# Optimization experiments

Measured on AMD Instinct MI355X. Metric: run time of the kernel, lower is better.

Reference implementation:

```python
import jax, jax.numpy as jnp
import numpy as np
import math

N, E, G = 10000, 100000, 500
HID, H = 128, 4
C = HID                      # out_channels per head (PyG TransformerConv)
NFREQ, NSPACE = 10, 3
EDIM = 2 * NFREQ * NSPACE    # 60 = dis_emb.dim
LAT, DIS = 6, 3
IN_DIM = HID + LAT + DIS     # 137
EPS = 1e-5


def _lin_init(k, fan_in, shape):
    b = 1.0 / math.sqrt(fan_in)
    return jax.random.uniform(k, shape, jnp.float32, -b, b)


def setup_inputs() -> dict:
    key = jax.random.key(0)
    ks = jax.random.split(key, 12)
    return dict(
        node_features=jax.random.normal(ks[0], (N, HID), jnp.float32),
        frac_coords=jax.random.uniform(ks[1], (N, DIS), jnp.float32),
        lattice_feats=jax.random.normal(ks[2], (G, LAT), jnp.float32),
        edge_index=jax.random.randint(ks[3], (2, E), 0, N),
        node2graph=jnp.sort(jax.random.randint(ks[4], (N,), 0, G)),
        frac_diff=jax.random.normal(ks[5], (E, DIS), jnp.float32) * 0.1,
        ln_gamma=jnp.ones((HID,), jnp.float32),
        ln_beta=jnp.zeros((HID,), jnp.float32),
        Wq=_lin_init(ks[6], IN_DIM, (IN_DIM, H * C)), bq=jnp.zeros((H * C,), jnp.float32),
        Wk=_lin_init(ks[7], IN_DIM, (IN_DIM, H * C)), bk=jnp.zeros((H * C,), jnp.float32),
        Wv=_lin_init(ks[8], IN_DIM, (IN_DIM, H * C)), bv=jnp.zeros((H * C,), jnp.float32),
        We=_lin_init(ks[9], EDIM, (EDIM, H * C)),
        Wskip=_lin_init(ks[10], IN_DIM, (IN_DIM, C)), bskip=jnp.zeros((C,), jnp.float32),
    )


def _sinusoids(frac_diff):
    # SinusoidsEmbedding: emb = x[...,None]*2*pi*arange(F); cat(sin, cos); detached
    freqs = 2.0 * jnp.pi * jnp.arange(NFREQ, dtype=jnp.float32)    # [F]
    emb = frac_diff[:, :, None] * freqs[None, None, :]             # [E,3,F]
    emb = emb.reshape(-1, NSPACE * NFREQ)                          # [E,30]
    return jnp.concatenate([jnp.sin(emb), jnp.cos(emb)], axis=-1)  # [E,60]


def _segment_softmax(scores, idx, num_segments):
    # softmax over variable-size neighborhoods grouped by target node idx
    m = jax.ops.segment_max(scores, idx, num_segments=num_segments)
    ex = jnp.exp(scores - m[idx])
    s = jax.ops.segment_sum(ex, idx, num_segments=num_segments)
    return ex / (s[idx] + 1e-16)


def reference(node_features, frac_coords, lattice_feats, edge_index, node2graph,
              frac_diff, ln_gamma, ln_beta, Wq, bq, Wk, bk, Wv, bv, We, Wskip, bskip):
    edge_emb = jax.lax.stop_gradient(_sinusoids(frac_diff))  # .detach() in original
    node_input = node_features
    # LayerNorm (biased variance, torch default)
    mu = node_features.mean(-1, keepdims=True)
    var = node_features.var(-1, keepdims=True)
    h = (node_features - mu) * jax.lax.rsqrt(var + EPS) * ln_gamma + ln_beta
    # gather per-graph lattice features to nodes, concat
    lat = lattice_feats.reshape(-1, LAT)[node2graph]                # [N,6]
    x = jnp.concatenate([h, lat, frac_coords], axis=1)              # [N,137]

    q = (x @ Wq + bq).reshape(N, H, C)
    k = (x @ Wk + bk).reshape(N, H, C)
    v = (x @ Wv + bv).reshape(N, H, C)
    e = (edge_emb @ We).reshape(E, H, C)                            # lin_edge (no bias)

    src, dst = edge_index[0], edge_index[1]  # message flows src -> dst (PyG default)
    k_e = k[src] + e                                                # [E,H,C]
    alpha = (q[dst] * k_e).sum(-1) / math.sqrt(C)                   # [E,H]
    alpha = _segment_softmax(alpha, dst, N)
    msg = (v[src] + e) * alpha[:, :, None]                          # [E,H,C]
    out = jax.ops.segment_sum(msg, dst, num_segments=N)             # [N,H,C]
    out = out.mean(axis=1)                                          # concat=False -> head mean
    out = out + (x @ Wskip + bskip)                                 # root skip connection
    return node_input + jax.nn.silu(out)
```

## Files before the change

kernel.cpp:

```cpp
#include <hip/hip_runtime.h>
#include <math.h>

#define N_NODES 10000
#define N_EDGES 100000
#define HIDDEN  128
#define NHEAD   4
#define CHAN    128
#define IN_DIM  137
#define KPAD    160
#define NCOLS   1904
#define NPAD    1920
#define LATD    6
#define DISD    3

#define PREP_BLOCKS 2500
#define TRANS_TILES 26
#define WQE_BLOCKS  150
#define WEBT_BLOCKS 128

#define SCAT_BLOCKS ((N_EDGES + 255) / 256)
#define GEMM_BX 15
#define GEMM_BY ((N_NODES + 63) / 64)

typedef __attribute__((ext_vector_type(8))) short short8v;
typedef __attribute__((ext_vector_type(4))) float float4v;
typedef __attribute__((ext_vector_type(2))) float float2v;

__device__ inline unsigned short f2bf(float f) {
    unsigned u = __float_as_uint(f);
    unsigned r = 0x7fffu + ((u >> 16) & 1u);
    return (unsigned short)((u + r) >> 16);
}
__device__ inline float bf2f(unsigned short u) {
    return __uint_as_float(((unsigned)u) << 16);
}

__global__ __launch_bounds__(256) void prep_weights_kernel(
    const float* __restrict__ nf, const float* __restrict__ frac,
    const float* __restrict__ lat, const int* __restrict__ n2g,
    const float* __restrict__ gamma, const float* __restrict__ beta,
    const float* __restrict__ Wq, const float* __restrict__ bq,
    const float* __restrict__ Wk, const float* __restrict__ bk,
    const float* __restrict__ Wv, const float* __restrict__ bv,
    const float* __restrict__ Wsk, const float* __restrict__ bsk,
    const float* __restrict__ We,
    unsigned short* __restrict__ xb, int* __restrict__ hist,
    unsigned short* __restrict__ wallT, float* __restrict__ bias_all,
    unsigned short* __restrict__ webt)
{
    __shared__ __align__(16) unsigned short Tlds[64 * 168];
    const int tid = threadIdx.x;

    if (blockIdx.x < PREP_BLOCKS) {
        int wave = tid >> 6;
        int lane = tid & 63;
        int n = blockIdx.x * 4 + wave;
        if (n >= N_NODES) return;

        float v0 = nf[n * HIDDEN + lane];
        float v1 = nf[n * HIDDEN + 64 + lane];
        float s  = v0 + v1;
        float sq = v0 * v0 + v1 * v1;
        #pragma unroll
        for (int m = 1; m < 64; m <<= 1) {
            s  += __shfl_xor(s, m);
            sq += __shfl_xor(sq, m);
        }
        float mean = s * (1.0f / 128.0f);
        float var  = sq * (1.0f / 128.0f) - mean * mean;
        float inv  = rsqrtf(var + 1e-5f);

        xb[n * KPAD + lane]      = f2bf((v0 - mean) * inv * gamma[lane]      + beta[lane]);
        xb[n * KPAD + 64 + lane] = f2bf((v1 - mean) * inv * gamma[64 + lane] + beta[64 + lane]);
        if (lane < LATD) xb[n * KPAD + HIDDEN + lane]        = f2bf(lat[n2g[n] * LATD + lane]);
        if (lane < DISD) xb[n * KPAD + HIDDEN + LATD + lane] = f2bf(frac[n * DISD + lane]);
        if (lane >= 41)  xb[n * KPAD + 96 + lane] = 0;
        if (lane == 0)   hist[n] = 0;
    } else if (blockIdx.x < PREP_BLOCKS + TRANS_TILES) {
        const int n0 = (blockIdx.x - PREP_BLOCKS) * 64;
        for (int i = tid; i < 160 * 64; i += 256) {
            const int k = i >> 6, n = i & 63;
            const int col = n0 + n;
            float val = 0.0f;
            if (k < IN_DIM) {
                if (col < 512)        val = Wq[(size_t)k * 512 + col];
                else if (col < 1024)  val = Wk[(size_t)k * 512 + (col - 512)];
                else if (col < 1536)  val = Wv[(size_t)k * 512 + (col - 1024)];
                else                  val = Wsk[(size_t)k * 128 + (col - 1536)];
            }
            Tlds[n * 168 + k] = f2bf(val);
        }
        __syncthreads();
        for (int i = tid; i < 64 * 20; i += 256) {
            const int n = i / 20, c8 = (i % 20) * 8;
            *reinterpret_cast<uint4*>(&wallT[(size_t)(n0 + n) * KPAD + c8]) =
                *reinterpret_cast<const uint4*>(&Tlds[n * 168 + c8]);
        }
        if (tid < 64) {
            const int col = n0 + tid;
            float b;
            if (col < 512)        b = bq[col];
            else if (col < 1024)  b = bk[col - 512];
            else if (col < 1536)  b = bv[col - 1024];
            else                  b = bsk[col - 1536];
            bias_all[col] = b;
        }
    } else if (blockIdx.x < PREP_BLOCKS + TRANS_TILES + WQE_BLOCKS) {
        int idx = (blockIdx.x - PREP_BLOCKS - TRANS_TILES) * 256 + tid;
        if (idx >= 240 * KPAD) return;
        int hj = idx / KPAD, k = idx % KPAD;
        int h = hj / 60, j = hj % 60;
        float s = 0.0f;
        if (k < IN_DIM) {
            #pragma unroll 4
            for (int c = 0; c < 128; ++c)
                s += Wq[(size_t)k * 512 + h * 128 + c] * We[(size_t)j * 512 + h * 128 + c];
        }
        wallT[(size_t)(1664 + hj) * KPAD + k] = f2bf(s);
        if (k == KPAD - 1) {
            float b = 0.0f;
            #pragma unroll 4
            for (int c = 0; c < 128; ++c)
                b += bq[h * 128 + c] * We[(size_t)j * 512 + h * 128 + c];
            bias_all[1664 + hj] = b;
        }
    } else {
        int g = (blockIdx.x - PREP_BLOCKS - TRANS_TILES - WQE_BLOCKS) * 256 + tid;
        if (g >= 4 * 128 * 64) return;
        int h = g >> 13, c = (g >> 6) & 127, j = g & 63;
        float v = (j < 60) ? We[(size_t)j * 512 + h * 128 + c] : 0.0f;
        webt[g] = f2bf(v);
    }
}

__global__ __launch_bounds__(256) void hist_kernel(
    const int* __restrict__ eidx, int* __restrict__ hist)
{
    int e = blockIdx.x * 256 + threadIdx.x;
    if (e < N_EDGES) atomicAdd(&hist[eidx[N_EDGES + e]], 1);
}

__global__ __launch_bounds__(1024) void scan_kernel(
    const int* __restrict__ hist, int* __restrict__ offsets, int* __restrict__ cursor)
{
    __shared__ int part[1024];
    const int t = threadIdx.x;
    const int base = t * 10;
    int loc[10];
    int s = 0;
    #pragma unroll
    for (int i = 0; i < 10; ++i) {
        int v = (base + i < N_NODES) ? hist[base + i] : 0;
        loc[i] = s; s += v;
    }
    part[t] = s;
    __syncthreads();
    for (int off = 1; off < 1024; off <<= 1) {
        int v = (t >= off) ? part[t - off] : 0;
        __syncthreads();
        part[t] += v;
        __syncthreads();
    }
    int pre = (t > 0) ? part[t - 1] : 0;
    #pragma unroll
    for (int i = 0; i < 10; ++i)
        if (base + i < N_NODES) {
            offsets[base + i] = pre + loc[i];
            cursor[base + i]  = pre + loc[i];
        }
    if (t == 1023) offsets[N_NODES] = part[1023];
}

__global__ __launch_bounds__(256) void gemm_scatter_kernel(
    const unsigned short* __restrict__ xb, const unsigned short* __restrict__ wallT,
    const float* __restrict__ bias_all,
    const int* __restrict__ eidx, const float* __restrict__ fdiff,
    int* __restrict__ cursor, int* __restrict__ sorted_src,
    float* __restrict__ sorted_fd,
    float* __restrict__ sq, unsigned short* __restrict__ qbuf,
    unsigned char* __restrict__ kvb)
{
    __shared__ __align__(16) unsigned short Alds[64 * 168];

    if (blockIdx.x < SCAT_BLOCKS) {
        int e = blockIdx.x * 256 + threadIdx.x;
        if (e >= N_EDGES) return;
        int src = eidx[e];
        int dst = eidx[N_EDGES + e];
        int pos = atomicAdd(&cursor[dst], 1);
        sorted_src[pos] = src;
        sorted_fd[pos * 3 + 0] = fdiff[e * 3 + 0];
        sorted_fd[pos * 3 + 1] = fdiff[e * 3 + 1];
        sorted_fd[pos * 3 + 2] = fdiff[e * 3 + 2];
        return;
    }

    const int bx   = blockIdx.x - SCAT_BLOCKS;
    const int row0 = (bx / GEMM_BX) * 64;
    const int col0 = (bx % GEMM_BX) * 128;
    const int tid  = threadIdx.x;

    for (int i = tid; i < 64 * 20; i += 256) {
        int r = i / 20, c8 = (i % 20) * 8;
        uint4 v = make_uint4(0u, 0u, 0u, 0u);
        if (row0 + r < N_NODES)
            v = *reinterpret_cast<const uint4*>(&xb[(size_t)(row0 + r) * KPAD + c8]);
        *reinterpret_cast<uint4*>(&Alds[r * 168 + c8]) = v;
    }
    __syncthreads();

    const int l   = tid & 63;
    const int wid = tid >> 6;
    const int wr  = (wid >> 1) * 32;
    const int wc  = (wid & 1) * 64;
    const int lr  = l & 15;
    const int lk  = (l >> 4) * 8;

    float4v acc[2][4];
    #pragma unroll
    for (int tr = 0; tr < 2; ++tr)
        #pragma unroll
        for (int tc = 0; tc < 4; ++tc)
            acc[tr][tc] = (float4v){0.0f, 0.0f, 0.0f, 0.0f};

    #pragma unroll
    for (int ks = 0; ks < 5; ++ks) {
        short8v a[2], b[4];
        #pragma unroll
        for (int t = 0; t < 2; ++t)
            a[t] = *reinterpret_cast<const short8v*>(&Alds[(wr + t * 16 + lr) * 168 + ks * 32 + lk]);
        #pragma unroll
        for (int t = 0; t < 4; ++t)
            b[t] = *reinterpret_cast<const short8v*>(
                &wallT[(size_t)(col0 + wc + t * 16 + lr) * KPAD + ks * 32 + lk]);
        #pragma unroll
        for (int tr = 0; tr < 2; ++tr)
            #pragma unroll
            for (int tc = 0; tc < 4; ++tc)
                acc[tr][tc] = __builtin_amdgcn_mfma_f32_16x16x32_bf16(a[tr], b[tc], acc[tr][tc], 0, 0, 0);
    }

    #pragma unroll
    for (int tr = 0; tr < 2; ++tr) {
        #pragma unroll
        for (int tc = 0; tc < 4; ++tc) {
            const int col  = col0 + wc + tc * 16 + lr;
            const float bias = bias_all[col];
            #pragma unroll
            for (int j = 0; j < 4; ++j) {
                const int row = row0 + wr + tr * 16 + (l >> 4) * 4 + j;
                if (row < N_NODES) {
                    float val = acc[tr][tc][j] + bias;
                    if (col < 512) {
                        qbuf[(size_t)row * 512 + col] = f2bf(val);
                    } else if (col < 1024) {
                        const int h = (col - 512) >> 7, ck = (col - 512) & 127;
                        int p = __builtin_amdgcn_cvt_pk_fp8_f32(val, val, 0, false);
                        kvb[((size_t)row * 4 + h) * 256 + ck] = (unsigned char)(p & 0xFF);
                    } else if (col < 1536) {
                        const int h = (col - 1024) >> 7, cv = (col - 1024) & 127;
                        int p = __builtin_amdgcn_cvt_pk_fp8_f32(val, val, 0, false);
                        kvb[((size_t)row * 4 + h) * 256 + 128 + cv] = (unsigned char)(p & 0xFF);
                    } else if (col < 1664) {
                        sq[(size_t)row * 384 + (col - 1536)] = val;
                    } else if (col < NCOLS) {
                        sq[(size_t)row * 384 + 128 + (col - 1664)] = val;
                    }
                }
            }
        }
    }
}

__global__ __launch_bounds__(256) void gather_kernel(
    const float* __restrict__ sq, const unsigned short* __restrict__ qbuf,
    const unsigned char* __restrict__ kvb,
    const int* __restrict__ offsets, const int* __restrict__ sorted_src,
    const float* __restrict__ sorted_fd,
    float* __restrict__ avbuf, unsigned short* __restrict__ aggbuf,
    float* __restrict__ sumwbuf)
{
    const int n    = blockIdx.x;
    const int h    = threadIdx.x >> 6;
    const int l    = threadIdx.x & 63;
    const int hl   = l & 31;
    const int half = l >> 5;
    const float TWO_PI = 6.283185307179586f;
    const float scale  = 0.08838834764831845f;

    const ushort4 qv = *reinterpret_cast<const ushort4*>(
        &qbuf[(size_t)n * 512 + h * 128 + 4 * hl]);
    const float q4x = bf2f(qv.x), q4y = bf2f(qv.y);
    const float q4z = bf2f(qv.z), q4w = bf2f(qv.w);
    const float qe_a = sq[(size_t)n * 384 + 128 + h * 60 + hl];
    const bool  v2ok = (hl < 28);
    const float qe_b = v2ok ? sq[(size_t)n * 384 + 128 + h * 60 + hl + 32] : 0.0f;

    const int   jj1  = (hl < 30) ? hl : hl - 30;
    const int   sd1  = jj1 / 10;
    const float fc1  = TWO_PI * (float)(jj1 % 10);
    const bool  sin1 = (hl < 30);
    const int   jj2  = hl + 2;
    const int   sd2  = v2ok ? (jj2 / 10) : 0;
    const float fc2  = v2ok ? TWO_PI * (float)(jj2 % 10) : 0.0f;

    float ax = 0.f, ay = 0.f, az = 0.f, aw = 0.f;
    float agg1 = 0.f, agg2 = 0.f, sumw = 0.f;
    const int e0 = offsets[n], e1 = offsets[n + 1];

    for (int base = e0; base < e1; base += 4) {
        const int eA = base + half;
        const int eB = base + half + 2;
        const bool okA = (eA < e1), okB = (eB < e1);
        const int iA = okA ? eA : e0;
        const int iB = okB ? eB : e0;
        const int srcA = sorted_src[iA];
        const int srcB = sorted_src[iB];
        const float fdA1 = sorted_fd[iA * 3 + sd1];
        const float fdA2 = sorted_fd[iA * 3 + sd2];
        const float fdB1 = sorted_fd[iB * 3 + sd1];
        const float fdB2 = sorted_fd[iB * 3 + sd2];
        const unsigned char* pA = kvb + ((size_t)srcA * 4 + h) * 256;
        const unsigned char* pB = kvb + ((size_t)srcB * 4 + h) * 256;
        const unsigned kAu = *reinterpret_cast<const unsigned*>(pA + 4 * hl);
        const unsigned vAu = *reinterpret_cast<const unsigned*>(pA + 128 + 4 * hl);
        const unsigned kBu = *reinterpret_cast<const unsigned*>(pB + 4 * hl);
        const unsigned vBu = *reinterpret_cast<const unsigned*>(pB + 128 + 4 * hl);

        const float eA1 = sin1 ? __sinf(fdA1 * fc1) : __cosf(fdA1 * fc1);
        const float eA2 = __cosf(fdA2 * fc2);
        const float eB1 = sin1 ? __sinf(fdB1 * fc1) : __cosf(fdB1 * fc1);
        const float eB2 = __cosf(fdB2 * fc2);

        const float2v kA01 = __builtin_amdgcn_cvt_pk_f32_fp8(kAu, false);
        const float2v kA23 = __builtin_amdgcn_cvt_pk_f32_fp8(kAu, true);
        const float2v kB01 = __builtin_amdgcn_cvt_pk_f32_fp8(kBu, false);
        const float2v kB23 = __builtin_amdgcn_cvt_pk_f32_fp8(kBu, true);

        float pAs = q4x * kA01[0] + q4y * kA01[1]
                  + q4z * kA23[0] + q4w * kA23[1]
                  + eA1 * qe_a + eA2 * qe_b;
        float pBs = q4x * kB01[0] + q4y * kB01[1]
                  + q4z * kB23[0] + q4w * kB23[1]
                  + eB1 * qe_a + eB2 * qe_b;
        #pragma unroll
        for (int m = 1; m <= 16; m <<= 1) {
            pAs += __shfl_xor(pAs, m);
            pBs += __shfl_xor(pBs, m);
        }
        const float wA = okA ? __expf(pAs * scale) : 0.0f;
        const float wB = okB ? __expf(pBs * scale) : 0.0f;
        sumw += wA + wB;

        const float2v vA01 = __builtin_amdgcn_cvt_pk_f32_fp8(vAu, false);
        const float2v vA23 = __builtin_amdgcn_cvt_pk_f32_fp8(vAu, true);
        const float2v vB01 = __builtin_amdgcn_cvt_pk_f32_fp8(vBu, false);
        const float2v vB23 = __builtin_amdgcn_cvt_pk_f32_fp8(vBu, true);
        ax += wA * vA01[0] + wB * vB01[0];
        ay += wA * vA01[1] + wB * vB01[1];
        az += wA * vA23[0] + wB * vB23[0];
        aw += wA * vA23[1] + wB * vB23[1];
        agg1 += wA * eA1 + wB * eB1;
        if (v2ok) agg2 += wA * eA2 + wB * eB2;
    }

    sumw += __shfl_xor(sumw, 32);
    ax += __shfl_xor(ax, 32);  ay += __shfl_xor(ay, 32);
    az += __shfl_xor(az, 32);  aw += __shfl_xor(aw, 32);
    agg1 += __shfl_xor(agg1, 32);
    agg2 += __shfl_xor(agg2, 32);

    if (half == 0) {
        float4 r;
        r.x = ax; r.y = ay; r.z = az; r.w = aw;
        *reinterpret_cast<float4*>(&avbuf[(size_t)n * 512 + h * 128 + 4 * hl]) = r;
        aggbuf[n * 256 + h * 64 + hl]      = f2bf(agg1);
        aggbuf[n * 256 + h * 64 + 32 + hl] = f2bf(agg2);
        if (hl == 0) sumwbuf[n * 4 + h] = sumw;
    }
}

__global__ __launch_bounds__(256) void corrfin_kernel(
    const unsigned short* __restrict__ webt, const unsigned short* __restrict__ aggbuf,
    const float* __restrict__ avbuf, const float* __restrict__ sumwbuf,
    const float* __restrict__ sq, const float* __restrict__ nf,
    float* __restrict__ out)
{
    const int node0 = blockIdx.x * 64;
    const int tid = threadIdx.x;
    const int l   = tid & 63;
    const int w   = tid >> 6;
    const int lr  = l & 15;
    const int lk  = (l >> 4) * 8;
    const int nbase = node0 + w * 16;

    float4v acc[4][8];
    #pragma unroll
    for (int h = 0; h < 4; ++h)
        #pragma unroll
        for (int nn = 0; nn < 8; ++nn)
            acc[h][nn] = (float4v){0.0f, 0.0f, 0.0f, 0.0f};

    const int arow = (nbase + lr < N_NODES) ? (nbase + lr) : 0;
    #pragma unroll
    for (int h = 0; h < 4; ++h) {
        #pragma unroll
        for (int ks = 0; ks < 2; ++ks) {
            const short8v a = *reinterpret_cast<const short8v*>(
                &aggbuf[(size_t)arow * 256 + h * 64 + ks * 32 + lk]);
            #pragma unroll
            for (int nn = 0; nn < 8; ++nn) {
                const short8v b = *reinterpret_cast<const short8v*>(
                    &webt[(size_t)(h * 128 + nn * 16 + lr) * 64 + ks * 32 + lk]);
                acc[h][nn] = __builtin_amdgcn_mfma_f32_16x16x32_bf16(a, b, acc[h][nn], 0, 0, 0);
            }
        }
    }

    float inv_sw[4][4];
    #pragma unroll
    for (int j = 0; j < 4; ++j) {
        const int node = nbase + (l >> 4) * 4 + j;
        const int nrd  = (node < N_NODES) ? node : 0;
        #pragma unroll
        for (int h = 0; h < 4; ++h)
            inv_sw[j][h] = 1.0f / (sumwbuf[nrd * 4 + h] + 1e-16f);
    }

    #pragma unroll
    for (int nn = 0; nn < 8; ++nn) {
        const int col = nn * 16 + lr;
        #pragma unroll
        for (int j = 0; j < 4; ++j) {
            const int node = nbase + (l >> 4) * 4 + j;
            if (node < N_NODES) {
                float z = 0.0f;
                #pragma unroll
                for (int h = 0; h < 4; ++h)
                    z += (avbuf[(size_t)node * 512 + h * 128 + col] + acc[h][nn][j])
                         * inv_sw[j][h];
                z = 0.25f * z + sq[(size_t)node * 384 + col];
                float si = z / (1.0f + __expf(-z));
                out[node * CHAN + col] = nf[node * CHAN + col] + si;
            }
        }
    }
}

extern "C" void kernel_launch(void* const* d_in, const int* in_sizes, int n_in,
                              void* d_out, int out_size, void* d_ws, size_t ws_size,
                              hipStream_t stream)
{
    const float* nf    = (const float*)d_in[0];
    const float* frac  = (const float*)d_in[1];
    const float* lat   = (const float*)d_in[2];
    const int*   eidx  = (const int*)  d_in[3];
    const int*   n2g   = (const int*)  d_in[4];
    const float* fdiff = (const float*)d_in[5];
    const float* gamma = (const float*)d_in[6];
    const float* beta  = (const float*)d_in[7];
    const float* Wq    = (const float*)d_in[8];
    const float* bq    = (const float*)d_in[9];
    const float* Wk    = (const float*)d_in[10];
    const float* bk    = (const float*)d_in[11];
    const float* Wv    = (const float*)d_in[12];
    const float* bv    = (const float*)d_in[13];
    const float* We    = (const float*)d_in[14];
    const float* Wsk   = (const float*)d_in[15];
    const float* bsk   = (const float*)d_in[16];
    float* out = (float*)d_out;

    float* sq        = (float*)d_ws;
    float* avbuf     = sq + (size_t)N_NODES * 384;
    float* sumwbuf   = avbuf + (size_t)N_NODES * 512;
    float* bias_all  = sumwbuf + (size_t)N_NODES * 4;
    float* sorted_fd = bias_all + NPAD;
    unsigned short* xb     = (unsigned short*)(sorted_fd + (size_t)N_EDGES * 3);
    unsigned short* wallT  = xb + (size_t)N_NODES * KPAD;
    unsigned short* webt   = wallT + (size_t)NPAD * KPAD;
    unsigned short* aggbuf = webt + 4 * 128 * 64;
    unsigned short* qbuf   = aggbuf + (size_t)N_NODES * 256;
    unsigned char*  kvb    = (unsigned char*)(qbuf + (size_t)N_NODES * 512);
    int* hist       = (int*)(kvb + (size_t)N_NODES * 4 * 256);
    int* offsets    = hist + N_NODES;
    int* cursor     = offsets + N_NODES + 1;
    int* sorted_src = cursor + N_NODES;

    prep_weights_kernel<<<PREP_BLOCKS + TRANS_TILES + WQE_BLOCKS + WEBT_BLOCKS,
                          256, 0, stream>>>(
        nf, frac, lat, n2g, gamma, beta,
        Wq, bq, Wk, bk, Wv, bv, Wsk, bsk, We,
        xb, hist, wallT, bias_all, webt);

    hist_kernel<<<(N_EDGES + 255) / 256, 256, 0, stream>>>(eidx, hist);
    scan_kernel<<<1, 1024, 0, stream>>>(hist, offsets, cursor);

    gemm_scatter_kernel<<<SCAT_BLOCKS + GEMM_BX * GEMM_BY, 256, 0, stream>>>(
        xb, wallT, bias_all, eidx, fdiff, cursor, sorted_src, sorted_fd,
        sq, qbuf, kvb);

    gather_kernel<<<N_NODES, 256, 0, stream>>>(
        sq, qbuf, kvb, offsets, sorted_src, sorted_fd, avbuf, aggbuf, sumwbuf);

    corrfin_kernel<<<(N_NODES + 63) / 64, 256, 0, stream>>>(
        webt, aggbuf, avbuf, sumwbuf, sq, nf, out);
}
```

Measured before the change: 134.3 us.

## Store GEMM operands in MFMA fragment layout and drop LDS staging

The prep kernel now writes the normalized node features and the concatenated weight matrix directly in MFMA 16x16x32 fragment order, so each lane's 8 bf16 values are contiguous. The GEMM kernel loads all A and B fragments straight from global memory into registers with coalesced 16-byte loads. This removes the shared-memory staging pass and its barrier. It also adds a launch-bounds occupancy hint. The cost is higher register pressure from holding all fragments at once, and the node-feature writes in the prep kernel become scattered.

```diff
diff --git a/kernel.cpp b/kernel.cpp
--- a/kernel.cpp
+++ b/kernel.cpp
@@ -21,6 +21,8 @@
 #define SCAT_BLOCKS ((N_EDGES + 255) / 256)
 #define GEMM_BX 15
 #define GEMM_BY ((N_NODES + 63) / 64)
+#define NR16    628
+#define FRAG_STRIDE (5 * 64 * 8)
 
 typedef __attribute__((ext_vector_type(8))) short short8v;
 typedef __attribute__((ext_vector_type(4))) float float4v;
@@ -33,6 +35,13 @@
 }
 __device__ inline float bf2f(unsigned short u) {
     return __uint_as_float(((unsigned)u) << 16);
+}
+__device__ inline size_t frag_off(int grp16, int ks, int lane) {
+    return (((size_t)grp16 * 5 + ks) * 64 + lane) * 8;
+}
+__device__ inline size_t frag_elem(int grp16, int lr, int k) {
+    const int ks = k >> 5, g = (k >> 3) & 3, e = k & 7;
+    return frag_off(grp16, ks, g * 16 + lr) + e;
 }
 
 __global__ __launch_bounds__(256) void prep_weights_kernel(
@@ -44,8 +53,8 @@
     const float* __restrict__ Wv, const float* __restrict__ bv,
     const float* __restrict__ Wsk, const float* __restrict__ bsk,
     const float* __restrict__ We,
-    unsigned short* __restrict__ xb, int* __restrict__ hist,
-    unsigned short* __restrict__ wallT, float* __restrict__ bias_all,
+    unsigned short* __restrict__ xfrag, int* __restrict__ hist,
+    unsigned short* __restrict__ wfrag, float* __restrict__ bias_all,
     unsigned short* __restrict__ webt)
 {
     __shared__ __align__(16) unsigned short Tlds[64 * 168];
@@ -70,12 +79,18 @@
         float var  = sq * (1.0f / 128.0f) - mean * mean;
         float inv  = rsqrtf(var + 1e-5f);
 
-        xb[n * KPAD + lane]      = f2bf((v0 - mean) * inv * gamma[lane]      + beta[lane]);
-        xb[n * KPAD + 64 + lane] = f2bf((v1 - mean) * inv * gamma[64 + lane] + beta[64 + lane]);
-        if (lane < LATD) xb[n * KPAD + HIDDEN + lane]        = f2bf(lat[n2g[n] * LATD + lane]);
-        if (lane < DISD) xb[n * KPAD + HIDDEN + LATD + lane] = f2bf(frac[n * DISD + lane]);
-        if (lane >= 41)  xb[n * KPAD + 96 + lane] = 0;
-        if (lane == 0)   hist[n] = 0;
+        const int r16 = n >> 4, lr = n & 15;
+        xfrag[frag_elem(r16, lr, lane)] =
+            f2bf((v0 - mean) * inv * gamma[lane] + beta[lane]);
+        xfrag[frag_elem(r16, lr, 64 + lane)] =
+            f2bf((v1 - mean) * inv * gamma[64 + lane] + beta[64 + lane]);
+        if (lane < LATD)
+            xfrag[frag_elem(r16, lr, HIDDEN + lane)] = f2bf(lat[n2g[n] * LATD + lane]);
+        if (lane < DISD)
+            xfrag[frag_elem(r16, lr, HIDDEN + LATD + lane)] = f2bf(frac[n * DISD + lane]);
+        if (lane >= 41)
+            xfrag[frag_elem(r16, lr, 96 + lane)] = 0;
+        if (lane == 0) hist[n] = 0;
     } else if (blockIdx.x < PREP_BLOCKS + TRANS_TILES) {
         const int n0 = (blockIdx.x - PREP_BLOCKS) * 64;
         for (int i = tid; i < 160 * 64; i += 256) {
@@ -91,10 +106,16 @@
             Tlds[n * 168 + k] = f2bf(val);
         }
         __syncthreads();
-        for (int i = tid; i < 64 * 20; i += 256) {
-            const int n = i / 20, c8 = (i % 20) * 8;
-            *reinterpret_cast<uint4*>(&wallT[(size_t)(n0 + n) * KPAD + c8]) =
-                *reinterpret_cast<const uint4*>(&Tlds[n * 168 + c8]);
+        for (int i = tid; i < 4 * 5 * 64; i += 256) {
+            const int lane = i & 63;
+            const int ks   = (i >> 6) % 5;
+            const int c16l = i / (5 * 64);
+            const int lr = lane & 15, g = lane >> 4;
+            const int lcol = c16l * 16 + lr;
+            const int k0 = ks * 32 + g * 8;
+            const short8v v = *reinterpret_cast<const short8v*>(&Tlds[lcol * 168 + k0]);
+            *reinterpret_cast<short8v*>(
+                &wfrag[frag_off((n0 >> 4) + c16l, ks, lane)]) = v;
         }
         if (tid < 64) {
             const int col = n0 + tid;
@@ -116,13 +137,14 @@
             for (int c = 0; c < 128; ++c)
                 s += Wq[(size_t)k * 512 + h * 128 + c] * We[(size_t)j * 512 + h * 128 + c];
         }
-        wallT[(size_t)(1664 + hj) * KPAD + k] = f2bf(s);
+        const int col = 1664 + hj;
+        wfrag[frag_elem(col >> 4, col & 15, k)] = f2bf(s);
         if (k == KPAD - 1) {
             float b = 0.0f;
             #pragma unroll 4
             for (int c = 0; c < 128; ++c)
                 b += bq[h * 128 + c] * We[(size_t)j * 512 + h * 128 + c];
-            bias_all[1664 + hj] = b;
+            bias_all[col] = b;
         }
     } else {
         int g = (blockIdx.x - PREP_BLOCKS - TRANS_TILES - WQE_BLOCKS) * 256 + tid;
@@ -171,8 +193,8 @@
     if (t == 1023) offsets[N_NODES] = part[1023];
 }
 
-__global__ __launch_bounds__(256) void gemm_scatter_kernel(
-    const unsigned short* __restrict__ xb, const unsigned short* __restrict__ wallT,
+__global__ __launch_bounds__(256, 2) void gemm_scatter_kernel(
+    const unsigned short* __restrict__ xfrag, const unsigned short* __restrict__ wfrag,
     const float* __restrict__ bias_all,
     const int* __restrict__ eidx, const float* __restrict__ fdiff,
     int* __restrict__ cursor, int* __restrict__ sorted_src,
@@ -180,8 +202,6 @@
     float* __restrict__ sq, unsigned short* __restrict__ qbuf,
     unsigned char* __restrict__ kvb)
 {
-    __shared__ __align__(16) unsigned short Alds[64 * 168];
-
     if (blockIdx.x < SCAT_BLOCKS) {
         int e = blockIdx.x * 256 + threadIdx.x;
         if (e >= N_EDGES) return;
@@ -199,22 +219,26 @@
     const int row0 = (bx / GEMM_BX) * 64;
     const int col0 = (bx % GEMM_BX) * 128;
     const int tid  = threadIdx.x;
-
-    for (int i = tid; i < 64 * 20; i += 256) {
-        int r = i / 20, c8 = (i % 20) * 8;
-        uint4 v = make_uint4(0u, 0u, 0u, 0u);
-        if (row0 + r < N_NODES)
-            v = *reinterpret_cast<const uint4*>(&xb[(size_t)(row0 + r) * KPAD + c8]);
-        *reinterpret_cast<uint4*>(&Alds[r * 168 + c8]) = v;
-    }
-    __syncthreads();
-
-    const int l   = tid & 63;
-    const int wid = tid >> 6;
-    const int wr  = (wid >> 1) * 32;
-    const int wc  = (wid & 1) * 64;
-    const int lr  = l & 15;
-    const int lk  = (l >> 4) * 8;
+    const int l    = tid & 63;
+    const int wid  = tid >> 6;
+    const int wr   = (wid >> 1) * 32;
+    const int wc   = (wid & 1) * 64;
+    const int lr   = l & 15;
+    const int r16  = (row0 + wr) >> 4;
+    const int c16  = (col0 + wc) >> 4;
+
+    short8v a[2][5], b[4][5];
+    #pragma unroll
+    for (int ks = 0; ks < 5; ++ks) {
+        #pragma unroll
+        for (int t = 0; t < 2; ++t)
+            a[t][ks] = *reinterpret_cast<const short8v*>(
+                &xfrag[frag_off(r16 + t, ks, l)]);
+        #pragma unroll
+        for (int t = 0; t < 4; ++t)
+            b[t][ks] = *reinterpret_cast<const short8v*>(
+                &wfrag[frag_off(c16 + t, ks, l)]);
+    }
 
     float4v acc[2][4];
     #pragma unroll
@@ -224,21 +248,13 @@
             acc[tr][tc] = (float4v){0.0f, 0.0f, 0.0f, 0.0f};
 
     #pragma unroll
-    for (int ks = 0; ks < 5; ++ks) {
-        short8v a[2], b[4];
-        #pragma unroll
-        for (int t = 0; t < 2; ++t)
-            a[t] = *reinterpret_cast<const short8v*>(&Alds[(wr + t * 16 + lr) * 168 + ks * 32 + lk]);
-        #pragma unroll
-        for (int t = 0; t < 4; ++t)
-            b[t] = *reinterpret_cast<const short8v*>(
-                &wallT[(size_t)(col0 + wc + t * 16 + lr) * KPAD + ks * 32 + lk]);
+    for (int ks = 0; ks < 5; ++ks)
         #pragma unroll
         for (int tr = 0; tr < 2; ++tr)
             #pragma unroll
             for (int tc = 0; tc < 4; ++tc)
-                acc[tr][tc] = __builtin_amdgcn_mfma_f32_16x16x32_bf16(a[tr], b[tc], acc[tr][tc], 0, 0, 0);
-    }
+                acc[tr][tc] = __builtin_amdgcn_mfma_f32_16x16x32_bf16(
+                    a[tr][ks], b[tc][ks], acc[tr][tc], 0, 0, 0);
 
     #pragma unroll
     for (int tr = 0; tr < 2; ++tr) {
@@ -475,9 +491,9 @@
     float* sumwbuf   = avbuf + (size_t)N_NODES * 512;
     float* bias_all  = sumwbuf + (size_t)N_NODES * 4;
     float* sorted_fd = bias_all + NPAD;
-    unsigned short* xb     = (unsigned short*)(sorted_fd + (size_t)N_EDGES * 3);
-    unsigned short* wallT  = xb + (size_t)N_NODES * KPAD;
-    unsigned short* webt   = wallT + (size_t)NPAD * KPAD;
+    unsigned short* xfrag  = (unsigned short*)(sorted_fd + (size_t)N_EDGES * 3);
+    unsigned short* wfrag  = xfrag + (size_t)NR16 * FRAG_STRIDE;
+    unsigned short* webt   = wfrag + (size_t)(NPAD / 16) * FRAG_STRIDE;
     unsigned short* aggbuf = webt + 4 * 128 * 64;
     unsigned short* qbuf   = aggbuf + (size_t)N_NODES * 256;
     unsigned char*  kvb    = (unsigned char*)(qbuf + (size_t)N_NODES * 512);
@@ -490,13 +506,13 @@
                           256, 0, stream>>>(
         nf, frac, lat, n2g, gamma, beta,
         Wq, bq, Wk, bk, Wv, bv, Wsk, bsk, We,
-        xb, hist, wallT, bias_all, webt);
+        xfrag, hist, wfrag, bias_all, webt);
 
     hist_kernel<<<(N_EDGES + 255) / 256, 256, 0, stream>>>(eidx, hist);
     scan_kernel<<<1, 1024, 0, stream>>>(hist, offsets, cursor);
 
     gemm_scatter_kernel<<<SCAT_BLOCKS + GEMM_BX * GEMM_BY, 256, 0, stream>>>(
-        xb, wallT, bias_all, eidx, fdiff, cursor, sorted_src, sorted_fd,
+        xfrag, wfrag, bias_all, eidx, fdiff, cursor, sorted_src, sorted_fd,
         sq, qbuf, kvb);
 
     gather_kernel<<<N_NODES, 256, 0, stream>>>(
```

Measured after the change: 130.2 us. 3.1% less time.
